# Kernel optimization log

Hardware: AMD Instinct MI355X
Metric: run time of the kernel (lower is better)

The kernel has to match this reference:

```python
import jax, jax.numpy as jnp
import numpy as np

B, N, K = 8, 2048, 8
POINT_DIM = 3
CTX_DIM = 256 + 256 + 3  # context_dim + cond_dim + 3 (time emb)
SLOPE = 0.2
LN_EPS = 1e-5


def _lin_init(key, fan_in, fan_out):
    w = jax.random.normal(key, (fan_in, fan_out), jnp.float32) / np.sqrt(fan_in)
    b = jnp.zeros((fan_out,), jnp.float32)
    return w, b


def setup_inputs() -> dict:
    key = jax.random.key(0)
    ks = jax.random.split(key, 12)
    x = jax.random.normal(ks[0], (B, N, POINT_DIM), jnp.float32)
    beta = jax.random.uniform(ks[1], (B,), jnp.float32)
    context = jax.random.normal(ks[2], (B, 256), jnp.float32)
    cond = jax.random.normal(ks[3], (B, 256), jnp.float32)
    W0, b0 = _lin_init(ks[4], POINT_DIM, 64)
    ln_g = jnp.ones((64,), jnp.float32)
    ln_b = jnp.zeros((64,), jnp.float32)
    W1, b1 = _lin_init(ks[5], 64 * 2 + CTX_DIM, 128)
    W2, b2 = _lin_init(ks[6], 128 * 2 + CTX_DIM, 256)
    W3, b3 = _lin_init(ks[7], 256 * 2 + CTX_DIM, 512)
    Wf1, bf1 = _lin_init(ks[8], 512, 256)
    Wf2, bf2 = _lin_init(ks[9], 256, POINT_DIM)
    return {"x": x, "beta": beta, "context": context, "cond": cond,
            "W0": W0, "b0": b0, "ln_g": ln_g, "ln_b": ln_b,
            "W1": W1, "b1": b1, "W2": W2, "b2": b2, "W3": W3, "b3": b3,
            "Wf1": Wf1, "bf1": bf1, "Wf2": Wf2, "bf2": bf2}


def _knn_idx(x):
    # x: (B,N,3) -> per-batch k-NN indices (B,N,K), self excluded
    sq = jnp.sum(x * x, axis=-1)  # (B,N)
    d = sq[:, :, None] + sq[:, None, :] - 2.0 * jnp.einsum('bnd,bmd->bnm', x, x)
    d = d + jnp.eye(N, dtype=x.dtype) * 1e10  # exclude self-loops
    _, idx = jax.lax.top_k(-d, K)  # k smallest distances
    return idx  # (B,N,K)


def _edge_conv(feat, idx, ctx, W, b):
    # feat: (B,N,D), idx: (B,N,K) int, ctx: (B,C)
    bidx = jnp.arange(B)[:, None, None]
    nb = feat[bidx, idx]                      # (B,N,K,D) gather neighbors
    center = jnp.broadcast_to(feat[:, :, None, :], nb.shape)
    c = jnp.broadcast_to(ctx[:, None, None, :], (B, N, K, ctx.shape[-1]))
    ef = jnp.concatenate([center, nb - center, c], axis=-1)  # (B,N,K,2D+C)
    h = jax.nn.leaky_relu(jnp.einsum('bnkf,fo->bnko', ef, W) + b, SLOPE)
    return jnp.max(h, axis=2)  # scatter_max over exactly K edges per node


def reference(x, beta, context, cond, W0, b0, ln_g, ln_b,
              W1, b1, W2, b2, W3, b3, Wf1, bf1, Wf2, bf2):
    time_emb = jnp.stack([beta, jnp.sin(beta), jnp.cos(beta)], axis=-1)  # (B,3)
    ctx = jnp.concatenate([time_emb, context, cond], axis=-1)            # (B,515)
    idx = _knn_idx(x)
    # init_mlp: Linear -> LeakyReLU(0.2) -> LayerNorm
    h = jax.nn.leaky_relu(x @ W0 + b0, SLOPE)
    mu = jnp.mean(h, axis=-1, keepdims=True)
    var = jnp.mean((h - mu) ** 2, axis=-1, keepdims=True)
    feat = (h - mu) * jax.lax.rsqrt(var + LN_EPS) * ln_g + ln_b  # (B,N,64)
    x1 = _edge_conv(feat, idx, ctx, W1, b1)
    x2 = _edge_conv(x1, idx, ctx, W2, b2)
    x3 = _edge_conv(x2, idx, ctx, W3, b3)
    out = jax.nn.leaky_relu(x3 @ Wf1 + bf1, SLOPE) @ Wf2 + bf2
    return x + out  # residual=True
```

## Files before the change

### kernel.cpp

```cpp
#include <hip/hip_runtime.h>
#include <cfloat>

constexpr int BATCH = 8, NPTS = 2048;
constexpr int M = BATCH * NPTS;
constexpr int CTXW = 515;

typedef __attribute__((ext_vector_type(8))) short bf16x8;
typedef __attribute__((ext_vector_type(4))) float f32x4;

__device__ __forceinline__ float lrelu(float v) { return v > 0.0f ? v : 0.2f * v; }
__device__ __forceinline__ float b2f(short u) {
    return __uint_as_float(((unsigned int)(unsigned short)u) << 16);
}
__device__ __forceinline__ short f2bf(float f) {
    unsigned int u = __float_as_uint(f);
    return (short)((u + 0x7FFF + ((u >> 16) & 1)) >> 16);
}

__global__ void zero1(int* p) { *p = 0; }

__global__ void build_ctx(const float* __restrict__ beta, const float* __restrict__ ctxv,
                          const float* __restrict__ cond, float* __restrict__ ctx) {
    int b = blockIdx.x;
    float be = beta[b];
    for (int i = threadIdx.x; i < CTXW; i += blockDim.x) {
        float v;
        if (i == 0) v = be;
        else if (i == 1) v = sinf(be);
        else if (i == 2) v = cosf(be);
        else if (i < 259) v = ctxv[b * 256 + (i - 3)];
        else v = cond[b * 256 + (i - 259)];
        ctx[b * CTXW + i] = v;
    }
}

__global__ __launch_bounds__(256) void ctx_bias_all(const float* __restrict__ ctx,
        const float* __restrict__ W1, const float* __restrict__ b1,
        const float* __restrict__ W2, const float* __restrict__ b2,
        const float* __restrict__ W3, const float* __restrict__ b3,
        float* __restrict__ bias1, float* __restrict__ bias2, float* __restrict__ bias3) {
    int b = blockIdx.y, blk = blockIdx.x;
    const float *W, *bv; float* out; int rowOff, F, fblk;
    if (blk < 2)      { W = W1; bv = b1; out = bias1; rowOff = 128; F = 128; fblk = blk; }
    else if (blk < 6) { W = W2; bv = b2; out = bias2; rowOff = 256; F = 256; fblk = blk - 2; }
    else              { W = W3; bv = b3; out = bias3; rowOff = 512; F = 512; fblk = blk - 6; }
    int fl = threadIdx.x >> 2, ks = threadIdx.x & 3;
    int f = fblk * 64 + fl;
    const float* c = ctx + b * CTXW;
    const float* w = W + (size_t)rowOff * F + f;
    float s = 0.f;
    for (int i = ks; i < CTXW; i += 4) s = fmaf(c[i], w[(size_t)i * F], s);
    s += __shfl_xor(s, 1);
    s += __shfl_xor(s, 2);
    if (ks == 0) out[(size_t)b * F + f] = s + bv[f];
}

__global__ void pack_all(const float* __restrict__ W1, const float* __restrict__ W2,
                         const float* __restrict__ W3, const float* __restrict__ Wf1,
                         short* __restrict__ W1p, short* __restrict__ W2p,
                         short* __restrict__ W3p, short* __restrict__ Wf1p) {
    int gid = blockIdx.x * 256 + threadIdx.x;
    if (gid < 16384) {
        int j = gid >> 6, k = gid & 63;
        float v = (j < 128) ? W1[(size_t)k * 128 + j] : W1[(size_t)(64 + k) * 128 + (j - 128)];
        W1p[gid] = f2bf(v);
    } else if (gid < 81920) {
        int g = gid - 16384; int j = g >> 7, k = g & 127;
        float v = (j < 256) ? W2[(size_t)k * 256 + j] : W2[(size_t)(128 + k) * 256 + (j - 256)];
        W2p[g] = f2bf(v);
    } else if (gid < 344064) {
        int g = gid - 81920; int j = g >> 8, k = g & 255;
        float v = (j < 512) ? W3[(size_t)k * 512 + j] : W3[(size_t)(256 + k) * 512 + (j - 512)];
        W3p[g] = f2bf(v);
    } else if (gid < 475136) {
        int g = gid - 344064; int f = g >> 9, k = g & 511;
        Wf1p[g] = f2bf(Wf1[(size_t)k * 256 + f]);
    }
}

__global__ __launch_bounds__(256, 1) void knn_sel(const float* __restrict__ x, int* __restrict__ idx,
                                                  int* __restrict__ flist, int* __restrict__ fcount) {
    __shared__ float4 xs4[NPTS];
    int b = blockIdx.y;
    const float* xb = x + (size_t)b * NPTS * 3;
    int tid = threadIdx.x;
    for (int i = tid; i < NPTS; i += 256)
        xs4[i] = make_float4(xb[i * 3], xb[i * 3 + 1], xb[i * 3 + 2], 0.f);
    __syncthreads();

    int w = tid >> 6, l = tid & 63;
    int n = blockIdx.x * 4 + w;
    float4 me = xs4[n];
    unsigned key[32];
    int selfrel = n - l;
#pragma unroll
    for (int j = 0; j < 32; ++j) {
        float4 c = xs4[j * 64 + l];
        float dx = me.x - c.x, dy = me.y - c.y, dz = me.z - c.z;
        float d = fmaf(dx, dx, fmaf(dy, dy, dz * dz));
        unsigned k = __float_as_uint(d);
        key[j] = (j * 64 == selfrel) ? 0xFFFFFFFFu : k;
    }

    int gn = b * NPTS + n;
    unsigned k8 = 0, k9 = 0;
    for (int p = 0; p < 9; ++p) {
        unsigned bk = 0xFFFFFFFFu;
        int bidx = 0x7FFFFFFF;
#pragma unroll
        for (int j = 0; j < 32; ++j) {
            bool t = key[j] < bk;
            bk = t ? key[j] : bk;
            bidx = t ? j * 64 + l : bidx;
        }
#pragma unroll
        for (int off = 32; off > 0; off >>= 1) {
            unsigned ok = __shfl_xor(bk, off);
            int oi = __shfl_xor(bidx, off);
            bool t = (ok < bk) || (ok == bk && oi < bidx);
            bk = t ? ok : bk;
            bidx = t ? oi : bidx;
        }
        int rel = bidx - l;
#pragma unroll
        for (int j = 0; j < 32; ++j)
            if (j * 64 == rel) key[j] = 0xFFFFFFFFu;
        if (p < 8) { if (l == p) idx[(size_t)gn * 8 + p] = b * NPTS + bidx; }
        if (p == 7) k8 = bk;
        if (p == 8) k9 = bk;
    }
    if (l == 0) {
        float d8 = __uint_as_float(k8), d9 = __uint_as_float(k9);
        float eps = 2e-5f * fmaxf(d9, 1.0f);
        if (d9 - d8 <= eps) {
            int pp = atomicAdd(fcount, 1);
            flist[pp] = gn;
        }
    }
}

__global__ __launch_bounds__(256, 1) void knn64_redo(const float* __restrict__ x, const int* __restrict__ flist,
                                                     const int* __restrict__ fcount, int* __restrict__ idx) {
    __shared__ double sd[2048];
    __shared__ int    si[2048];
    __shared__ double s2d[128];
    __shared__ int    s2i[128];
    int cnt = *fcount;
    int tid = threadIdx.x;
    for (int it = blockIdx.x; it < cnt; it += gridDim.x) {
        int gn = flist[it];
        int b = gn >> 11, n = gn & 2047;
        const float* xb = x + (size_t)b * NPTS * 3;
        float n0 = xb[n * 3], n1 = xb[n * 3 + 1], n2 = xb[n * 3 + 2];
        double sqn = ((double)n0 * n0 + (double)n1 * n1) + (double)n2 * n2;
        double bd[8]; int bidx[8];
#pragma unroll
        for (int k = 0; k < 8; ++k) { bd[k] = DBL_MAX; bidx[k] = 0; }
        for (int j = 0; j < 8; ++j) {
            int m = tid * 8 + j;
            float c0 = xb[m * 3], c1 = xb[m * 3 + 1], c2 = xb[m * 3 + 2];
            double sqm = ((double)c0 * c0 + (double)c1 * c1) + (double)c2 * c2;
            double dot = ((double)n0 * c0 + (double)n1 * c1) + (double)n2 * c2;
            double d = (sqn + sqm) - 2.0 * dot;
            if (m == n) continue;
            if (d < bd[7]) {
                double cd = d; int ci = m;
#pragma unroll
                for (int q = 0; q < 8; ++q) {
                    if (cd < bd[q]) {
                        double td = bd[q]; bd[q] = cd; cd = td;
                        int ti = bidx[q]; bidx[q] = ci; ci = ti;
                    }
                }
            }
        }
#pragma unroll
        for (int k = 0; k < 8; ++k) { sd[tid * 8 + k] = bd[k]; si[tid * 8 + k] = bidx[k]; }
        __syncthreads();
        if (tid < 16) {
            double fb[8]; int fi[8];
#pragma unroll
            for (int k = 0; k < 8; ++k) { fb[k] = DBL_MAX; fi[k] = 0; }
            for (int t = tid * 16; t < tid * 16 + 16; ++t) {
                for (int k = 0; k < 8; ++k) {
                    double d = sd[t * 8 + k];
                    if (d >= fb[7]) break;
                    int ci = si[t * 8 + k];
                    double cd = d;
#pragma unroll
                    for (int q = 0; q < 8; ++q) {
                        if (cd < fb[q]) {
                            double td = fb[q]; fb[q] = cd; cd = td;
                            int ti = fi[q]; fi[q] = ci; ci = ti;
                        }
                    }
                }
            }
#pragma unroll
            for (int k = 0; k < 8; ++k) { s2d[tid * 8 + k] = fb[k]; s2i[tid * 8 + k] = fi[k]; }
        }
        __syncthreads();
        if (tid == 0) {
            double fb[8]; int fi[8];
#pragma unroll
            for (int k = 0; k < 8; ++k) { fb[k] = DBL_MAX; fi[k] = 0; }
            for (int t = 0; t < 16; ++t) {
                for (int k = 0; k < 8; ++k) {
                    double d = s2d[t * 8 + k];
                    if (d >= fb[7]) break;
                    int ci = s2i[t * 8 + k];
                    double cd = d;
#pragma unroll
                    for (int q = 0; q < 8; ++q) {
                        if (cd < fb[q]) {
                            double td = fb[q]; fb[q] = cd; cd = td;
                            int ti = fi[q]; fi[q] = ci; ci = ti;
                        }
                    }
                }
            }
#pragma unroll
            for (int k = 0; k < 8; ++k) idx[(size_t)gn * 8 + k] = b * NPTS + fi[k];
        }
        __syncthreads();
    }
}

__global__ __launch_bounds__(256) void init_ln(const float* __restrict__ x, const float* __restrict__ W0,
                                               const float* __restrict__ b0, const float* __restrict__ g,
                                               const float* __restrict__ be, short* __restrict__ feat) {
    int t = blockIdx.x * 256 + threadIdx.x;
    int node = t >> 6, c = t & 63;
    const float* xp = x + (size_t)node * 3;
    float h = fmaf(xp[0], W0[c], fmaf(xp[1], W0[64 + c], fmaf(xp[2], W0[128 + c], b0[c])));
    h = lrelu(h);
    float s = h;
#pragma unroll
    for (int o = 32; o > 0; o >>= 1) s += __shfl_xor(s, o);
    float mu = s * (1.0f / 64.0f);
    float tt = h - mu;
    float q = tt * tt;
#pragma unroll
    for (int o = 32; o > 0; o >>= 1) q += __shfl_xor(q, o);
    float var = q * (1.0f / 64.0f);
    feat[t] = f2bf(tt * rsqrtf(var + 1e-5f) * g[c] + be[c]);
}

__global__ __launch_bounds__(256) void gemm_mfma(const short* __restrict__ A, const short* __restrict__ Bt,
                                                 short* __restrict__ C, int N, int K,
                                                 const float* __restrict__ bias, int fuse_lrelu) {
    __shared__ __align__(16) char Asw[128 * 128];
    __shared__ __align__(16) char Bsw[128 * 128];
    int tid = threadIdx.x;
    int lane = tid & 63, wid = tid >> 6;
    int wm = wid >> 1, wn = wid & 1;
    int mBase = blockIdx.x * 128, nBase = blockIdx.y * 128;
    int lo = lane & 15, hi = lane >> 4;

    f32x4 acc[4][4];
#pragma unroll
    for (int i = 0; i < 4; ++i)
#pragma unroll
        for (int j = 0; j < 4; ++j) acc[i][j] = (f32x4){0.f, 0.f, 0.f, 0.f};

    int sr = tid >> 3;
    int sc = tid & 7;

    for (int k0 = 0; k0 < K; k0 += 64) {
        bf16x8 av[4], bv[4];
#pragma unroll
        for (int i = 0; i < 4; ++i) {
            int row = i * 32 + sr;
            av[i] = *(const bf16x8*)(A + (size_t)(mBase + row) * K + k0 + sc * 8);
            bv[i] = *(const bf16x8*)(Bt + (size_t)(nBase + row) * K + k0 + sc * 8);
        }
        __syncthreads();
#pragma unroll
        for (int i = 0; i < 4; ++i) {
            int row = i * 32 + sr;
            int off = row * 128 + ((sc * 16) ^ ((row & 7) << 4));
            *(bf16x8*)(Asw + off) = av[i];
            *(bf16x8*)(Bsw + off) = bv[i];
        }
        __syncthreads();
#pragma unroll
        for (int kk = 0; kk < 2; ++kk) {
            bf16x8 af[4], bfr[4];
            int kb = kk * 64 + hi * 16;
#pragma unroll
            for (int q = 0; q < 4; ++q) {
                int rowA = wm * 64 + q * 16 + lo;
                af[q] = *(const bf16x8*)(Asw + rowA * 128 + (kb ^ ((rowA & 7) << 4)));
                int rowB = wn * 64 + q * 16 + lo;
                bfr[q] = *(const bf16x8*)(Bsw + rowB * 128 + (kb ^ ((rowB & 7) << 4)));
            }
#pragma unroll
            for (int fm = 0; fm < 4; ++fm)
#pragma unroll
                for (int fn = 0; fn < 4; ++fn)
                    acc[fm][fn] = __builtin_amdgcn_mfma_f32_16x16x32_bf16(af[fm], bfr[fn], acc[fm][fn], 0, 0, 0);
        }
    }

#pragma unroll
    for (int fm = 0; fm < 4; ++fm) {
        int m0 = mBase + wm * 64 + fm * 16 + hi * 4;
#pragma unroll
        for (int fn = 0; fn < 4; ++fn) {
            int n = nBase + wn * 64 + fn * 16 + lo;
            float bb = bias ? bias[n] : 0.0f;
#pragma unroll
            for (int rr = 0; rr < 4; ++rr) {
                float v = acc[fm][fn][rr] + bb;
                if (fuse_lrelu) v = lrelu(v);
                C[(size_t)(m0 + rr) * N + n] = f2bf(v);
            }
        }
    }
}

__global__ __launch_bounds__(256) void edge_max(const short* __restrict__ UV, const int* __restrict__ idx,
                                                const float* __restrict__ bias, short* __restrict__ out,
                                                int F, int lf ) {
    int gid = blockIdx.x * 256 + threadIdx.x;
    int n = gid >> lf;
    int f = (gid & ((F >> 3) - 1)) << 3;
    int b = n >> 11;
    int F2 = F << 1;
    const short* base = UV + (size_t)n * F2;
    bf16x8 u8 = *(const bf16x8*)(base + f);
    bf16x8 v8 = *(const bf16x8*)(base + F + f);
    const int* ip = idx + (size_t)n * 8;
    float mx[8];
#pragma unroll
    for (int j = 0; j < 8; ++j) mx[j] = -FLT_MAX;
#pragma unroll
    for (int k = 0; k < 8; ++k) {
        bf16x8 w8 = *(const bf16x8*)(UV + (size_t)ip[k] * F2 + F + f);
#pragma unroll
        for (int j = 0; j < 8; ++j) mx[j] = fmaxf(mx[j], b2f(w8[j]));
    }
    const float* bp = bias + (size_t)b * F + f;
    bf16x8 z;
#pragma unroll
    for (int j = 0; j < 8; ++j)
        z[j] = f2bf(lrelu(b2f(u8[j]) - b2f(v8[j]) + bp[j] + mx[j]));
    *(bf16x8*)(out + (size_t)n * F + f) = z;
}

__global__ __launch_bounds__(256) void final_out(const short* __restrict__ hf, const float* __restrict__ Wf2,
                                                 const float* __restrict__ bf2, const float* __restrict__ x,
                                                 float* __restrict__ out) {
    int n = blockIdx.x * 256 + threadIdx.x;
    const short* h = hf + (size_t)n * 256;
    float s0 = bf2[0], s1 = bf2[1], s2 = bf2[2];
    for (int k8 = 0; k8 < 32; ++k8) {
        bf16x8 hv = *(const bf16x8*)(h + k8 * 8);
        const float* w = Wf2 + k8 * 24;
#pragma unroll
        for (int j = 0; j < 8; ++j) {
            float hh = b2f(hv[j]);
            s0 = fmaf(hh, w[j * 3 + 0], s0);
            s1 = fmaf(hh, w[j * 3 + 1], s1);
            s2 = fmaf(hh, w[j * 3 + 2], s2);
        }
    }
    out[n * 3 + 0] = x[n * 3 + 0] + s0;
    out[n * 3 + 1] = x[n * 3 + 1] + s1;
    out[n * 3 + 2] = x[n * 3 + 2] + s2;
}

extern "C" void kernel_launch(void* const* d_in, const int* in_sizes, int n_in,
                              void* d_out, int out_size, void* d_ws, size_t ws_size,
                              hipStream_t stream) {
    const float* x    = (const float*)d_in[0];
    const float* beta = (const float*)d_in[1];
    const float* ctxv = (const float*)d_in[2];
    const float* cond = (const float*)d_in[3];
    const float* W0   = (const float*)d_in[4];
    const float* b0   = (const float*)d_in[5];
    const float* ln_g = (const float*)d_in[6];
    const float* ln_b = (const float*)d_in[7];
    const float* W1   = (const float*)d_in[8];
    const float* b1   = (const float*)d_in[9];
    const float* W2   = (const float*)d_in[10];
    const float* b2   = (const float*)d_in[11];
    const float* W3   = (const float*)d_in[12];
    const float* b3   = (const float*)d_in[13];
    const float* Wf1  = (const float*)d_in[14];
    const float* bf1  = (const float*)d_in[15];
    const float* Wf2  = (const float*)d_in[16];
    const float* bf2  = (const float*)d_in[17];
    float* out = (float*)d_out;

    char* ws = (char*)d_ws;
    size_t off = 0;
    auto alloc = [&](size_t bytes) -> void* {
        void* p = ws + off;
        off += bytes;
        off = (off + 511) & ~(size_t)511;
        return p;
    };

    int*   idx    = (int*)alloc((size_t)M * 8 * 4);
    int*   fcount = (int*)alloc(4);
    int*   flist  = (int*)alloc((size_t)M * 4);
    float* ctx   = (float*)alloc((size_t)BATCH * CTXW * 4);
    float* bias1 = (float*)alloc((size_t)BATCH * 128 * 4);
    float* bias2 = (float*)alloc((size_t)BATCH * 256 * 4);
    float* bias3 = (float*)alloc((size_t)BATCH * 512 * 4);
    short* W1p   = (short*)alloc((size_t)256 * 64 * 2);
    short* W2p   = (short*)alloc((size_t)512 * 128 * 2);
    short* W3p   = (short*)alloc((size_t)1024 * 256 * 2);
    short* Wf1p  = (short*)alloc((size_t)256 * 512 * 2);
    short* R1    = (short*)alloc((size_t)M * 1024 * 2);
    short* R2    = (short*)alloc((size_t)M * 512 * 2);
    short* R3    = (short*)alloc((size_t)M * 256 * 2);
    short* R4    = (short*)alloc((size_t)M * 256 * 2);

    short* feat0 = R1;
    short* UV1 = R2;  short* x1 = R3;
    short* UV2 = R2;  short* x2 = R4;
    short* UV3 = R1;  short* x3 = R2;
    short* hf  = R3;

    zero1<<<1, 1, 0, stream>>>(fcount);
    build_ctx<<<BATCH, 256, 0, stream>>>(beta, ctxv, cond, ctx);
    ctx_bias_all<<<dim3(14, BATCH), 256, 0, stream>>>(ctx, W1, b1, W2, b2, W3, b3, bias1, bias2, bias3);
    pack_all<<<(475136 + 255) / 256, 256, 0, stream>>>(W1, W2, W3, Wf1, W1p, W2p, W3p, Wf1p);

    knn_sel<<<dim3(NPTS / 4, BATCH), 256, 0, stream>>>(x, idx, flist, fcount);
    init_ln<<<M * 64 / 256, 256, 0, stream>>>(x, W0, b0, ln_g, ln_b, feat0);
    knn64_redo<<<256, 256, 0, stream>>>(x, flist, fcount, idx);

    gemm_mfma<<<dim3(M / 128, 2), 256, 0, stream>>>(feat0, W1p, UV1, 256, 64, nullptr, 0);
    edge_max<<<M * 16 / 256, 256, 0, stream>>>(UV1, idx, bias1, x1, 128, 4);

    gemm_mfma<<<dim3(M / 128, 4), 256, 0, stream>>>(x1, W2p, UV2, 512, 128, nullptr, 0);
    edge_max<<<M * 32 / 256, 256, 0, stream>>>(UV2, idx, bias2, x2, 256, 5);

    gemm_mfma<<<dim3(M / 128, 8), 256, 0, stream>>>(x2, W3p, UV3, 1024, 256, nullptr, 0);
    edge_max<<<M * 64 / 256, 256, 0, stream>>>(UV3, idx, bias3, x3, 512, 6);

    gemm_mfma<<<dim3(M / 128, 2), 256, 0, stream>>>(x3, Wf1p, hf, 256, 512, bf1, 1);

    final_out<<<M / 256, 256, 0, stream>>>(hf, Wf2, bf2, x, out);
}
```

Measured before the change: 261.3 us.

## Pack kNN keys with indices, use direct global-to-LDS loads in GEMM, remap edge blocks

The kNN selection packs the point index into the low 11 bits of the distance key, so each of the 9 passes becomes a tree min plus a wave min instead of carrying a separate index. It also relaxes the tie threshold that sends points to the double-precision redo. The GEMM loads tiles straight into swizzled LDS with global_load_lds instead of staging them through registers. edge_max remaps block IDs into an interleaved order, and the zero kernel is folded into build_ctx. Truncating the distance mantissa reduces key precision, which can send more points to the redo path, and the tile loads are no longer overlapped with register staging.

```diff
diff --git a/kernel.cpp b/kernel.cpp
--- a/kernel.cpp
+++ b/kernel.cpp
@@ -16,12 +16,17 @@
     unsigned int u = __float_as_uint(f);
     return (short)((u + 0x7FFF + ((u >> 16) & 1)) >> 16);
 }
-
-__global__ void zero1(int* p) { *p = 0; }
+__device__ __forceinline__ void gl16(const void* g, void* l) {
+    __builtin_amdgcn_global_load_lds((const __attribute__((address_space(1))) unsigned int*)g,
+                                     (__attribute__((address_space(3))) unsigned int*)l,
+                                     16, 0, 0);
+}
 
 __global__ void build_ctx(const float* __restrict__ beta, const float* __restrict__ ctxv,
-                          const float* __restrict__ cond, float* __restrict__ ctx) {
+                          const float* __restrict__ cond, float* __restrict__ ctx,
+                          int* __restrict__ fcount) {
     int b = blockIdx.x;
+    if (b == 0 && threadIdx.x == 0) *fcount = 0;
     float be = beta[b];
     for (int i = threadIdx.x; i < CTXW; i += blockDim.x) {
         float v;
@@ -78,8 +83,8 @@
     }
 }
 
-__global__ __launch_bounds__(256, 1) void knn_sel(const float* __restrict__ x, int* __restrict__ idx,
-                                                  int* __restrict__ flist, int* __restrict__ fcount) {
+__global__ __launch_bounds__(256) void knn_sel(const float* __restrict__ x, int* __restrict__ idx,
+                                               int* __restrict__ flist, int* __restrict__ fcount) {
     __shared__ float4 xs4[NPTS];
     int b = blockIdx.y;
     const float* xb = x + (size_t)b * NPTS * 3;
@@ -92,55 +97,54 @@
     int n = blockIdx.x * 4 + w;
     float4 me = xs4[n];
     unsigned key[32];
-    int selfrel = n - l;
 #pragma unroll
     for (int j = 0; j < 32; ++j) {
-        float4 c = xs4[j * 64 + l];
+        int m = j * 64 + l;
+        float4 c = xs4[m];
         float dx = me.x - c.x, dy = me.y - c.y, dz = me.z - c.z;
         float d = fmaf(dx, dx, fmaf(dy, dy, dz * dz));
-        unsigned k = __float_as_uint(d);
-        key[j] = (j * 64 == selfrel) ? 0xFFFFFFFFu : k;
-    }
-
-    int gn = b * NPTS + n;
-    unsigned k8 = 0, k9 = 0;
+        unsigned k = (__float_as_uint(d) & 0xFFFFF800u) | (unsigned)m;
+        key[j] = (m == n) ? 0xFFFFFFFFu : k;
+    }
+
+    unsigned win[9];
+#pragma unroll
     for (int p = 0; p < 9; ++p) {
-        unsigned bk = 0xFFFFFFFFu;
-        int bidx = 0x7FFFFFFF;
-#pragma unroll
-        for (int j = 0; j < 32; ++j) {
-            bool t = key[j] < bk;
-            bk = t ? key[j] : bk;
-            bidx = t ? j * 64 + l : bidx;
-        }
-#pragma unroll
-        for (int off = 32; off > 0; off >>= 1) {
-            unsigned ok = __shfl_xor(bk, off);
-            int oi = __shfl_xor(bidx, off);
-            bool t = (ok < bk) || (ok == bk && oi < bidx);
-            bk = t ? ok : bk;
-            bidx = t ? oi : bidx;
-        }
-        int rel = bidx - l;
-#pragma unroll
-        for (int j = 0; j < 32; ++j)
-            if (j * 64 == rel) key[j] = 0xFFFFFFFFu;
-        if (p < 8) { if (l == p) idx[(size_t)gn * 8 + p] = b * NPTS + bidx; }
-        if (p == 7) k8 = bk;
-        if (p == 8) k9 = bk;
+        unsigned m16[16], m8[8], m4[4], m2[2];
+#pragma unroll
+        for (int j = 0; j < 16; ++j) m16[j] = min(key[2 * j], key[2 * j + 1]);
+#pragma unroll
+        for (int j = 0; j < 8; ++j) m8[j] = min(m16[2 * j], m16[2 * j + 1]);
+#pragma unroll
+        for (int j = 0; j < 4; ++j) m4[j] = min(m8[2 * j], m8[2 * j + 1]);
+        m2[0] = min(m4[0], m4[1]); m2[1] = min(m4[2], m4[3]);
+        unsigned bk = min(m2[0], m2[1]);
+#pragma unroll
+        for (int off = 32; off > 0; off >>= 1)
+            bk = min(bk, (unsigned)__shfl_xor((unsigned)bk, off));
+        win[p] = bk;
+        if (p < 8) {
+#pragma unroll
+            for (int j = 0; j < 32; ++j)
+                key[j] = (key[j] == bk) ? 0xFFFFFFFFu : key[j];
+        }
     }
     if (l == 0) {
-        float d8 = __uint_as_float(k8), d9 = __uint_as_float(k9);
-        float eps = 2e-5f * fmaxf(d9, 1.0f);
-        if (d9 - d8 <= eps) {
+        int gn = b * NPTS + n;
+#pragma unroll
+        for (int p = 0; p < 8; ++p)
+            idx[(size_t)gn * 8 + p] = b * NPTS + (int)(win[p] & 2047u);
+        float d8 = __uint_as_float(win[7] & 0xFFFFF800u);
+        float d9 = __uint_as_float(win[8] & 0xFFFFF800u);
+        if (d9 - d8 <= 1e-3f * d9) {
             int pp = atomicAdd(fcount, 1);
             flist[pp] = gn;
         }
     }
 }
 
-__global__ __launch_bounds__(256, 1) void knn64_redo(const float* __restrict__ x, const int* __restrict__ flist,
-                                                     const int* __restrict__ fcount, int* __restrict__ idx) {
+__global__ __launch_bounds__(256) void knn64_redo(const float* __restrict__ x, const int* __restrict__ flist,
+                                                  const int* __restrict__ fcount, int* __restrict__ idx) {
     __shared__ double sd[2048];
     __shared__ int    si[2048];
     __shared__ double s2d[128];
@@ -263,24 +267,19 @@
 #pragma unroll
         for (int j = 0; j < 4; ++j) acc[i][j] = (f32x4){0.f, 0.f, 0.f, 0.f};
 
-    int sr = tid >> 3;
-    int sc = tid & 7;
+    int w8 = lane >> 3, c8 = lane & 7;
+    int swz = ((c8 ^ w8) << 4);
+    const char* Ab = (const char*)A;
+    const char* Bb = (const char*)Bt;
+    size_t strideB = (size_t)K * 2;
 
     for (int k0 = 0; k0 < K; k0 += 64) {
-        bf16x8 av[4], bv[4];
+        __syncthreads();
 #pragma unroll
         for (int i = 0; i < 4; ++i) {
-            int row = i * 32 + sr;
-            av[i] = *(const bf16x8*)(A + (size_t)(mBase + row) * K + k0 + sc * 8);
-            bv[i] = *(const bf16x8*)(Bt + (size_t)(nBase + row) * K + k0 + sc * 8);
-        }
-        __syncthreads();
-#pragma unroll
-        for (int i = 0; i < 4; ++i) {
-            int row = i * 32 + sr;
-            int off = row * 128 + ((sc * 16) ^ ((row & 7) << 4));
-            *(bf16x8*)(Asw + off) = av[i];
-            *(bf16x8*)(Bsw + off) = bv[i];
+            int r0 = wid * 32 + i * 8;
+            gl16(Ab + (size_t)(mBase + r0 + w8) * strideB + k0 * 2 + swz, Asw + r0 * 128);
+            gl16(Bb + (size_t)(nBase + r0 + w8) * strideB + k0 * 2 + swz, Bsw + r0 * 128);
         }
         __syncthreads();
 #pragma unroll
@@ -322,7 +321,10 @@
 __global__ __launch_bounds__(256) void edge_max(const short* __restrict__ UV, const int* __restrict__ idx,
                                                 const float* __restrict__ bias, short* __restrict__ out,
                                                 int F, int lf ) {
-    int gid = blockIdx.x * 256 + threadIdx.x;
+    int nblk = gridDim.x;
+    int bid = blockIdx.x;
+    int bid2 = (bid & 7) * (nblk >> 3) + (bid >> 3);
+    int gid = bid2 * 256 + threadIdx.x;
     int n = gid >> lf;
     int f = (gid & ((F >> 3) - 1)) << 3;
     int b = n >> 11;
@@ -424,8 +426,7 @@
     short* UV3 = R1;  short* x3 = R2;
     short* hf  = R3;
 
-    zero1<<<1, 1, 0, stream>>>(fcount);
-    build_ctx<<<BATCH, 256, 0, stream>>>(beta, ctxv, cond, ctx);
+    build_ctx<<<BATCH, 256, 0, stream>>>(beta, ctxv, cond, ctx, fcount);
     ctx_bias_all<<<dim3(14, BATCH), 256, 0, stream>>>(ctx, W1, b1, W2, b2, W3, b3, bias1, bias2, bias3);
     pack_all<<<(475136 + 255) / 256, 256, 0, stream>>>(W1, W2, W3, Wf1, W1p, W2p, W3p, Wf1p);
 
```

Result: faster. 219.1 us (-16.2%).
